# Kernel tuning notes

Measured on AMD Instinct MI355X. Metric: run time of the kernel, lower is better.

Reference implementation:

```python
import jax, jax.numpy as jnp
import numpy as np

N = 1048576      # n_samples
DIM = 3
SPLIT = DIM // 2        # 1
H = 64                  # hidden_dim
NF = 8                  # num_flows
OUT2 = (DIM - SPLIT)    # 2 (scale/shift each)


def setup_inputs() -> dict:
    key = jax.random.key(0)
    ks = jax.random.split(key, 9)
    eps = jax.random.normal(ks[0], (N, DIM), dtype=jnp.float32)
    # Cholesky-style lower-triangular param; positive-ish diagonal so cov is PD
    L_tril = jnp.tril(jax.random.normal(ks[1], (DIM, DIM), dtype=jnp.float32) * 0.1
                      + jnp.eye(DIM, dtype=jnp.float32) * np.sqrt(0.1).astype(np.float32))
    base_mean = jax.random.normal(ks[2], (DIM,), dtype=jnp.float32) * 0.1
    # stacked per-flow MLP weights (torch Linear convention: y = x @ W.T + b)
    W1 = jax.random.normal(ks[3], (NF, H, SPLIT), dtype=jnp.float32) * 0.5
    b1 = jax.random.normal(ks[4], (NF, H), dtype=jnp.float32) * 0.1
    W2 = jax.random.normal(ks[5], (NF, H, H), dtype=jnp.float32) * 0.05
    b2 = jax.random.normal(ks[6], (NF, H), dtype=jnp.float32) * 0.1
    W3 = jax.random.normal(ks[7], (NF, OUT2 * 2, H), dtype=jnp.float32) * 0.05
    b3 = jax.random.normal(ks[8], (NF, OUT2 * 2), dtype=jnp.float32) * 0.05
    return {"L_tril": L_tril, "base_mean": base_mean,
            "W1": W1, "b1": b1, "W2": W2, "b2": b2, "W3": W3, "b3": b3,
            "eps": eps}


def reference(L_tril, base_mean, W1, b1, W2, b2, W3, b3, eps):
    # base distribution sample via Cholesky of cov = L L^T
    L = jnp.tril(L_tril) + jnp.eye(DIM, dtype=L_tril.dtype) * 1e-6
    cov = L @ L.T
    Lc = jnp.linalg.cholesky(cov)
    z = base_mean + eps @ Lc.T                       # [N, 3]

    def coupling(carry, params):
        z, ld = carry
        w1, bb1, w2, bb2, w3, bb3 = params
        z1, z2 = z[:, :SPLIT], z[:, SPLIT:]
        h = jax.nn.relu(z1 @ w1.T + bb1)             # [N, 64]
        h = jax.nn.relu(h @ w2.T + bb2)              # [N, 64]
        p = h @ w3.T + bb3                           # [N, 4]
        scale = jnp.tanh(p[:, :OUT2])                # [N, 2]
        shift = p[:, OUT2:]
        z2t = z2 * jnp.exp(scale) + shift
        z = jnp.concatenate([z1, z2t], axis=1)
        ld = ld + scale.sum(axis=1)
        return (z, ld), None

    ld0 = jnp.zeros(eps.shape[0], dtype=z.dtype)
    (z, log_det), _ = jax.lax.scan(coupling, (z, ld0), (W1, b1, W2, b2, W3, b3))

    # exp-transform columns 1 and 2 (positivity constraint)
    z_transformed = z.at[:, 1].set(jnp.exp(z[:, 1])).at[:, 2].set(jnp.exp(z[:, 2]))
    log_det_total = log_det + z[:, 1].sum() + z[:, 2].sum()
    return z_transformed, log_det_total
```

## Files before the change

### kernel.cpp

```cpp
#include <hip/hip_runtime.h>

#define NS 1048576
#define NFLOW 8
#define HD 64
#define GT 2048
#define PTS 8

#define EMIN -7.5f
#define ESPAN 15.0f
#define GDEL (ESPAN / (float)(GT - 1))
#define GINV ((float)(GT - 1) / ESPAN)

#define WS_AB   64
#define WS_LD   (WS_AB + GT * 16)
#define WS_PART ((WS_LD + GT * 4 + 63) & ~63)

__device__ __forceinline__ void cholesky9(const float* __restrict__ L_tril, float* d) {
    double l00 = (double)L_tril[0] + 1e-6;
    double l10 = (double)L_tril[3];
    double l11 = (double)L_tril[4] + 1e-6;
    double l20 = (double)L_tril[6];
    double l21 = (double)L_tril[7];
    double l22 = (double)L_tril[8] + 1e-6;
    double c00 = l00 * l00;
    double c10 = l10 * l00;
    double c11 = l10 * l10 + l11 * l11;
    double c20 = l20 * l00;
    double c21 = l20 * l10 + l21 * l11;
    double c22 = l20 * l20 + l21 * l21 + l22 * l22;
    double d00 = sqrt(c00);
    double d10 = c10 / d00;
    double d20 = c20 / d00;
    double d11 = sqrt(c11 - d10 * d10);
    double d21 = (c21 - d20 * d10) / d11;
    double d22 = sqrt(c22 - d20 * d20 - d21 * d21);
    d[0] = (float)d00; d[1] = (float)d10; d[2] = (float)d11;
    d[3] = (float)d20; d[4] = (float)d21; d[5] = (float)d22;
}

__global__ void __launch_bounds__(512) k_build(
    const float* __restrict__ L_tril, const float* __restrict__ bm,
    const float* __restrict__ W1, const float* __restrict__ b1,
    const float* __restrict__ W2, const float* __restrict__ b2,
    const float* __restrict__ W3, const float* __restrict__ b3,
    char* __restrict__ ws) {
    const int CHUNKS = GT / PTS;
    int t = blockIdx.x / CHUNKS;
    int chunk = blockIdx.x % CHUNKS;
    int tid = threadIdx.x;
    int pg = tid >> 6;
    int j = tid & 63;
    int p = chunk * PTS + pg;

    __shared__ float w2s[HD * 65];
    __shared__ float w1s[HD], b1s[HD], b2s[HD], w3s[4 * HD];
    __shared__ float h1s[PTS][HD];

    for (int idx = tid; idx < HD * HD; idx += 512)
        w2s[(idx >> 6) * 65 + (idx & 63)] = W2[t * HD * HD + idx];
    if (tid < HD) {
        w1s[tid] = W1[t * HD + tid];
        b1s[tid] = b1[t * HD + tid];
        b2s[tid] = b2[t * HD + tid];
    }
    if (tid < 4 * HD) w3s[tid] = W3[t * 4 * HD + tid];
    __syncthreads();

    float Lc00 = fabsf(L_tril[0] + 1e-6f);
    float z0 = fmaf(Lc00, fmaf(GDEL, (float)p, EMIN), bm[0]);
    float h1 = fmaf(z0, w1s[j], b1s[j]);
    h1s[pg][j] = h1 > 0.f ? h1 : 0.f;
    __syncthreads();

    float a0 = 0.f, a1 = 0.f;
    const float* row = &w2s[j * 65];
    const float* hh = h1s[pg];
#pragma unroll
    for (int k = 0; k < HD; k += 2) {
        a0 = fmaf(row[k], hh[k], a0);
        a1 = fmaf(row[k + 1], hh[k + 1], a1);
    }
    float acc = b2s[j] + a0 + a1;
    float h2 = acc > 0.f ? acc : 0.f;

    float c0 = w3s[j] * h2;
    float c1 = w3s[HD + j] * h2;
    float c2 = w3s[2 * HD + j] * h2;
    float c3 = w3s[3 * HD + j] * h2;
#pragma unroll
    for (int o = 32; o > 0; o >>= 1) {
        c0 += __shfl_xor(c0, o);
        c1 += __shfl_xor(c1, o);
        c2 += __shfl_xor(c2, o);
        c3 += __shfl_xor(c3, o);
    }
    if (j == 0) {
        const float* bb3 = b3 + t * 4;
        ((float4*)(ws + WS_PART))[t * GT + p] =
            make_float4(tanhf(c0 + bb3[0]), tanhf(c1 + bb3[1]), c2 + bb3[2], c3 + bb3[3]);
    }
}

__global__ void __launch_bounds__(256) k_compose(const float* __restrict__ L_tril,
                                                 const float* __restrict__ bm,
                                                 char* __restrict__ ws) {
    int p = blockIdx.x * blockDim.x + threadIdx.x;
    const float4* partial = (const float4*)(ws + WS_PART);
    float A1 = 1.f, B1 = 0.f, A2 = 1.f, B2 = 0.f, LD = 0.f;
#pragma unroll
    for (int t = 0; t < NFLOW; t++) {
        float4 v = partial[t * GT + p];
        float a1 = expf(v.x), a2 = expf(v.y);
        A1 *= a1; B1 = fmaf(B1, a1, v.z);
        A2 *= a2; B2 = fmaf(B2, a2, v.w);
        LD += v.x + v.y;
    }
    ((float4*)(ws + WS_AB))[p] = make_float4(A1, B1, A2, B2);
    ((float*)(ws + WS_LD))[p] = LD;
    if (p == 0) {
        *(double*)ws = 0.0;
        float d[6];
        cholesky9(L_tril, d);
        float* pr = (float*)(ws + 16);
        pr[0] = bm[0]; pr[1] = bm[1]; pr[2] = bm[2];
        pr[3] = d[0]; pr[4] = d[1]; pr[5] = d[2];
        pr[6] = d[3]; pr[7] = d[4]; pr[8] = d[5];
    }
}

__global__ void __launch_bounds__(256) k_main(const float4* __restrict__ eps4,
                                              char* __restrict__ ws,
                                              float* __restrict__ out) {
    int i = blockIdx.x * blockDim.x + threadIdx.x;
    const float* pr = (const float*)(ws + 16);
    float bm0 = pr[0], bm1 = pr[1], bm2 = pr[2];
    float Lc00 = pr[3], Lc10 = pr[4], Lc11 = pr[5], Lc20 = pr[6], Lc21 = pr[7], Lc22 = pr[8];
    const float4* tabAB = (const float4*)(ws + WS_AB);
    const float* tabLD = (const float*)(ws + WS_LD);

    float4 a = eps4[3 * i], b = eps4[3 * i + 1], c = eps4[3 * i + 2];
    float e0[4] = {a.x, a.w, b.z, c.y};
    float e1[4] = {a.y, b.x, b.w, c.z};
    float e2[4] = {a.z, b.y, c.x, c.w};
    float zo[12], ld[4];
    float lsum = 0.f;
#pragma unroll
    for (int s = 0; s < 4; s++) {
        float z0 = fmaf(Lc00, e0[s], bm0);
        float z1 = fmaf(Lc11, e1[s], fmaf(Lc10, e0[s], bm1));
        float z2 = fmaf(Lc22, e2[s], fmaf(Lc21, e1[s], fmaf(Lc20, e0[s], bm2)));
        float u = (e0[s] - EMIN) * GINV;
        u = fminf(fmaxf(u, 0.f), (float)(GT - 1));
        int g = (int)u;
        if (g > GT - 2) g = GT - 2;
        float f = u - (float)g;
        float4 t0 = tabAB[g], t1 = tabAB[g + 1];
        float A1 = fmaf(f, t1.x - t0.x, t0.x);
        float B1 = fmaf(f, t1.y - t0.y, t0.y);
        float A2 = fmaf(f, t1.z - t0.z, t0.z);
        float B2 = fmaf(f, t1.w - t0.w, t0.w);
        float l0 = tabLD[g];
        float LD = fmaf(f, tabLD[g + 1] - l0, l0);
        float z1f = fmaf(z1, A1, B1);
        float z2f = fmaf(z2, A2, B2);
        zo[3 * s]     = z0;
        zo[3 * s + 1] = expf(z1f);
        zo[3 * s + 2] = expf(z2f);
        ld[s] = LD;
        lsum += z1f + z2f;
    }
    float4* o4 = (float4*)out;
    o4[3 * i]     = make_float4(zo[0], zo[1], zo[2], zo[3]);
    o4[3 * i + 1] = make_float4(zo[4], zo[5], zo[6], zo[7]);
    o4[3 * i + 2] = make_float4(zo[8], zo[9], zo[10], zo[11]);
    ((float4*)(out + 3 * (size_t)NS))[i] = make_float4(ld[0], ld[1], ld[2], ld[3]);

    for (int o = 32; o > 0; o >>= 1) lsum += __shfl_down(lsum, o);
    __shared__ float sred[4];
    int lane = threadIdx.x & 63, wid = threadIdx.x >> 6;
    if (lane == 0) sred[wid] = lsum;
    __syncthreads();
    if (threadIdx.x == 0) {
        double tot = (double)sred[0] + (double)sred[1] + (double)sred[2] + (double)sred[3];
        atomicAdd((double*)ws, tot);
    }
}

__global__ void __launch_bounds__(256) k_adds(float* __restrict__ out,
                                              const char* __restrict__ ws) {
    int i = blockIdx.x * blockDim.x + threadIdx.x;
    float S = (float)(*(const double*)ws);
    float4* p = (float4*)(out + 3 * (size_t)NS);
    float4 v = p[i];
    v.x += S; v.y += S; v.z += S; v.w += S;
    p[i] = v;
}

extern "C" void kernel_launch(void* const* d_in, const int* in_sizes, int n_in,
                              void* d_out, int out_size, void* d_ws, size_t ws_size,
                              hipStream_t stream) {
    const float* L_tril = (const float*)d_in[0];
    const float* bm     = (const float*)d_in[1];
    const float* W1     = (const float*)d_in[2];
    const float* b1     = (const float*)d_in[3];
    const float* W2     = (const float*)d_in[4];
    const float* b2     = (const float*)d_in[5];
    const float* W3     = (const float*)d_in[6];
    const float* b3     = (const float*)d_in[7];
    const float* eps    = (const float*)d_in[8];
    char* ws = (char*)d_ws;
    float* out = (float*)d_out;

    k_build<<<NFLOW * (GT / PTS), 512, 0, stream>>>(L_tril, bm, W1, b1, W2, b2, W3, b3, ws);
    k_compose<<<GT / 256, 256, 0, stream>>>(L_tril, bm, ws);
    k_main<<<NS / 4 / 256, 256, 0, stream>>>((const float4*)eps, ws, out);
    k_adds<<<NS / 4 / 256, 256, 0, stream>>>(out, ws);
}
```

Before: 118.0 us.

## Fuse flow composition into build kernel and fold log-det add via grid barrier

The per-flow build and compose kernels become one kernel in which each block loops over all 8 flows and composes the affine coefficients in registers, so the partial-table round trip and one launch go away. The separate k_adds pass is removed. k_main now does a software grid barrier: it atomically counts finished blocks, spins until all 1024 have added to the global sum, then writes log-det with the sum already added. This saves a full read-modify-write of the 4 MB log-det array. The barrier assumes all blocks are co-resident (launch_bounds 256,4 is meant to help with that), and the build kernel now launches fewer blocks that each do serial per-flow work.

```diff
diff --git a/kernel.cpp b/kernel.cpp
--- a/kernel.cpp
+++ b/kernel.cpp
@@ -5,15 +5,15 @@
 #define HD 64
 #define GT 2048
 #define PTS 8
+#define NBLK (NS / 4 / 256)
 
 #define EMIN -7.5f
 #define ESPAN 15.0f
 #define GDEL (ESPAN / (float)(GT - 1))
 #define GINV ((float)(GT - 1) / ESPAN)
 
-#define WS_AB   64
-#define WS_LD   (WS_AB + GT * 16)
-#define WS_PART ((WS_LD + GT * 4 + 63) & ~63)
+#define WS_AB 64
+#define WS_LD (WS_AB + GT * 16)
 
 __device__ __forceinline__ void cholesky9(const float* __restrict__ L_tril, float* d) {
     double l00 = (double)L_tril[0] + 1e-6;
@@ -44,81 +44,77 @@
     const float* __restrict__ W2, const float* __restrict__ b2,
     const float* __restrict__ W3, const float* __restrict__ b3,
     char* __restrict__ ws) {
-    const int CHUNKS = GT / PTS;
-    int t = blockIdx.x / CHUNKS;
-    int chunk = blockIdx.x % CHUNKS;
     int tid = threadIdx.x;
     int pg = tid >> 6;
     int j = tid & 63;
-    int p = chunk * PTS + pg;
+    int p = blockIdx.x * PTS + pg;
 
     __shared__ float w2s[HD * 65];
     __shared__ float w1s[HD], b1s[HD], b2s[HD], w3s[4 * HD];
     __shared__ float h1s[PTS][HD];
 
-    for (int idx = tid; idx < HD * HD; idx += 512)
-        w2s[(idx >> 6) * 65 + (idx & 63)] = W2[t * HD * HD + idx];
-    if (tid < HD) {
-        w1s[tid] = W1[t * HD + tid];
-        b1s[tid] = b1[t * HD + tid];
-        b2s[tid] = b2[t * HD + tid];
-    }
-    if (tid < 4 * HD) w3s[tid] = W3[t * 4 * HD + tid];
-    __syncthreads();
-
     float Lc00 = fabsf(L_tril[0] + 1e-6f);
     float z0 = fmaf(Lc00, fmaf(GDEL, (float)p, EMIN), bm[0]);
-    float h1 = fmaf(z0, w1s[j], b1s[j]);
-    h1s[pg][j] = h1 > 0.f ? h1 : 0.f;
-    __syncthreads();
-
-    float a0 = 0.f, a1 = 0.f;
-    const float* row = &w2s[j * 65];
-    const float* hh = h1s[pg];
+
+    float A1 = 1.f, B1 = 0.f, A2 = 1.f, B2 = 0.f, LD = 0.f;
+
+    for (int t = 0; t < NFLOW; t++) {
+        __syncthreads();
+        for (int idx = tid; idx < HD * HD; idx += 512)
+            w2s[(idx >> 6) * 65 + (idx & 63)] = W2[t * HD * HD + idx];
+        if (tid < HD) {
+            w1s[tid] = W1[t * HD + tid];
+            b1s[tid] = b1[t * HD + tid];
+            b2s[tid] = b2[t * HD + tid];
+        }
+        if (tid < 4 * HD) w3s[tid] = W3[t * 4 * HD + tid];
+        __syncthreads();
+
+        float h1 = fmaf(z0, w1s[j], b1s[j]);
+        h1s[pg][j] = h1 > 0.f ? h1 : 0.f;
+        __syncthreads();
+
+        float a0 = 0.f, a1 = 0.f, a2 = 0.f, a3 = 0.f;
+        const float* row = &w2s[j * 65];
+        const float* hh = h1s[pg];
 #pragma unroll
-    for (int k = 0; k < HD; k += 2) {
-        a0 = fmaf(row[k], hh[k], a0);
-        a1 = fmaf(row[k + 1], hh[k + 1], a1);
-    }
-    float acc = b2s[j] + a0 + a1;
-    float h2 = acc > 0.f ? acc : 0.f;
-
-    float c0 = w3s[j] * h2;
-    float c1 = w3s[HD + j] * h2;
-    float c2 = w3s[2 * HD + j] * h2;
-    float c3 = w3s[3 * HD + j] * h2;
+        for (int k = 0; k < HD; k += 4) {
+            a0 = fmaf(row[k],     hh[k],     a0);
+            a1 = fmaf(row[k + 1], hh[k + 1], a1);
+            a2 = fmaf(row[k + 2], hh[k + 2], a2);
+            a3 = fmaf(row[k + 3], hh[k + 3], a3);
+        }
+        float acc = b2s[j] + ((a0 + a1) + (a2 + a3));
+        float h2 = acc > 0.f ? acc : 0.f;
+
+        float c0 = w3s[j] * h2;
+        float c1 = w3s[HD + j] * h2;
+        float c2 = w3s[2 * HD + j] * h2;
+        float c3 = w3s[3 * HD + j] * h2;
 #pragma unroll
-    for (int o = 32; o > 0; o >>= 1) {
-        c0 += __shfl_xor(c0, o);
-        c1 += __shfl_xor(c1, o);
-        c2 += __shfl_xor(c2, o);
-        c3 += __shfl_xor(c3, o);
-    }
+        for (int o = 32; o > 0; o >>= 1) {
+            c0 += __shfl_xor(c0, o);
+            c1 += __shfl_xor(c1, o);
+            c2 += __shfl_xor(c2, o);
+            c3 += __shfl_xor(c3, o);
+        }
+        float s0  = tanhf(c0 + b3[t * 4 + 0]);
+        float s1  = tanhf(c1 + b3[t * 4 + 1]);
+        float sh0 = c2 + b3[t * 4 + 2];
+        float sh1 = c3 + b3[t * 4 + 3];
+        float e1 = expf(s0), e2 = expf(s1);
+        A1 *= e1; B1 = fmaf(B1, e1, sh0);
+        A2 *= e2; B2 = fmaf(B2, e2, sh1);
+        LD += s0 + s1;
+    }
+
     if (j == 0) {
-        const float* bb3 = b3 + t * 4;
-        ((float4*)(ws + WS_PART))[t * GT + p] =
-            make_float4(tanhf(c0 + bb3[0]), tanhf(c1 + bb3[1]), c2 + bb3[2], c3 + bb3[3]);
-    }
-}
-
-__global__ void __launch_bounds__(256) k_compose(const float* __restrict__ L_tril,
-                                                 const float* __restrict__ bm,
-                                                 char* __restrict__ ws) {
-    int p = blockIdx.x * blockDim.x + threadIdx.x;
-    const float4* partial = (const float4*)(ws + WS_PART);
-    float A1 = 1.f, B1 = 0.f, A2 = 1.f, B2 = 0.f, LD = 0.f;
-#pragma unroll
-    for (int t = 0; t < NFLOW; t++) {
-        float4 v = partial[t * GT + p];
-        float a1 = expf(v.x), a2 = expf(v.y);
-        A1 *= a1; B1 = fmaf(B1, a1, v.z);
-        A2 *= a2; B2 = fmaf(B2, a2, v.w);
-        LD += v.x + v.y;
-    }
-    ((float4*)(ws + WS_AB))[p] = make_float4(A1, B1, A2, B2);
-    ((float*)(ws + WS_LD))[p] = LD;
-    if (p == 0) {
+        ((float4*)(ws + WS_AB))[p] = make_float4(A1, B1, A2, B2);
+        ((float*)(ws + WS_LD))[p] = LD;
+    }
+    if (tid == 0 && blockIdx.x == 0) {
         *(double*)ws = 0.0;
+        *(unsigned*)(ws + 8) = 0u;
         float d[6];
         cholesky9(L_tril, d);
         float* pr = (float*)(ws + 16);
@@ -128,9 +124,9 @@
     }
 }
 
-__global__ void __launch_bounds__(256) k_main(const float4* __restrict__ eps4,
-                                              char* __restrict__ ws,
-                                              float* __restrict__ out) {
+__global__ void __launch_bounds__(256, 4) k_main(const float4* __restrict__ eps4,
+                                                 char* __restrict__ ws,
+                                                 float* __restrict__ out) {
     int i = blockIdx.x * blockDim.x + threadIdx.x;
     const float* pr = (const float*)(ws + 16);
     float bm0 = pr[0], bm1 = pr[1], bm2 = pr[2];
@@ -173,27 +169,29 @@
     o4[3 * i]     = make_float4(zo[0], zo[1], zo[2], zo[3]);
     o4[3 * i + 1] = make_float4(zo[4], zo[5], zo[6], zo[7]);
     o4[3 * i + 2] = make_float4(zo[8], zo[9], zo[10], zo[11]);
-    ((float4*)(out + 3 * (size_t)NS))[i] = make_float4(ld[0], ld[1], ld[2], ld[3]);
 
     for (int o = 32; o > 0; o >>= 1) lsum += __shfl_down(lsum, o);
     __shared__ float sred[4];
+    __shared__ float sbc;
     int lane = threadIdx.x & 63, wid = threadIdx.x >> 6;
     if (lane == 0) sred[wid] = lsum;
     __syncthreads();
+    double* Sacc = (double*)ws;
+    unsigned* cnt = (unsigned*)(ws + 8);
     if (threadIdx.x == 0) {
         double tot = (double)sred[0] + (double)sred[1] + (double)sred[2] + (double)sred[3];
-        atomicAdd((double*)ws, tot);
-    }
-}
-
-__global__ void __launch_bounds__(256) k_adds(float* __restrict__ out,
-                                              const char* __restrict__ ws) {
-    int i = blockIdx.x * blockDim.x + threadIdx.x;
-    float S = (float)(*(const double*)ws);
-    float4* p = (float4*)(out + 3 * (size_t)NS);
-    float4 v = p[i];
-    v.x += S; v.y += S; v.z += S; v.w += S;
-    p[i] = v;
+        atomicAdd(Sacc, tot);
+        __threadfence();
+        __hip_atomic_fetch_add(cnt, 1u, __ATOMIC_RELEASE, __HIP_MEMORY_SCOPE_AGENT);
+        while (__hip_atomic_load(cnt, __ATOMIC_ACQUIRE, __HIP_MEMORY_SCOPE_AGENT) < NBLK)
+            __builtin_amdgcn_s_sleep(1);
+        double Sv = __hip_atomic_load(Sacc, __ATOMIC_ACQUIRE, __HIP_MEMORY_SCOPE_AGENT);
+        sbc = (float)Sv;
+    }
+    __syncthreads();
+    float S = sbc;
+    ((float4*)(out + 3 * (size_t)NS))[i] =
+        make_float4(ld[0] + S, ld[1] + S, ld[2] + S, ld[3] + S);
 }
 
 extern "C" void kernel_launch(void* const* d_in, const int* in_sizes, int n_in,
@@ -211,8 +209,6 @@
     char* ws = (char*)d_ws;
     float* out = (float*)d_out;
 
-    k_build<<<NFLOW * (GT / PTS), 512, 0, stream>>>(L_tril, bm, W1, b1, W2, b2, W3, b3, ws);
-    k_compose<<<GT / 256, 256, 0, stream>>>(L_tril, bm, ws);
-    k_main<<<NS / 4 / 256, 256, 0, stream>>>((const float4*)eps, ws, out);
-    k_adds<<<NS / 4 / 256, 256, 0, stream>>>(out, ws);
-}
+    k_build<<<GT / PTS, 512, 0, stream>>>(L_tril, bm, W1, b1, W2, b2, W3, b3, ws);
+    k_main<<<NBLK, 256, 0, stream>>>((const float4*)eps, ws, out);
+}
```

Result: slower. 278.8 us (+136.2%).
